# Kernel tuning notes

Measured on AMD Instinct MI355X. Metric: run time of the kernel, lower is better.

Reference implementation:

```python
import jax, jax.numpy as jnp
import numpy as np

D_MODEL = 2048
N_HEADS = 16
HEAD_DIM = D_MODEL // N_HEADS
ROPE_BASE = 10000.0
B, T = 2, 2048


def setup_inputs() -> dict:
    key = jax.random.key(0)
    k1, k2, k3 = jax.random.split(key, 3)
    s_in = 1.0 / np.sqrt(D_MODEL)
    x = jax.random.normal(k1, (B, T, D_MODEL), dtype=jnp.float32)
    Wqkv = jax.random.normal(k2, (3 * D_MODEL, D_MODEL), dtype=jnp.float32) * s_in
    bqkv = jnp.zeros((3 * D_MODEL,), dtype=jnp.float32)
    Wo = jax.random.normal(k3, (D_MODEL, D_MODEL), dtype=jnp.float32) * s_in
    bo = jnp.zeros((D_MODEL,), dtype=jnp.float32)
    return {"x": x, "Wqkv": Wqkv, "bqkv": bqkv, "Wo": Wo, "bo": bo}


def _rotate_half(x):
    # [x1,x2,x3,x4] -> [-x2,x1,-x4,x3] (interleaved pairs)
    x_even = x[..., 0::2]
    x_odd = x[..., 1::2]
    return jnp.stack((-x_odd, x_even), axis=-1).reshape(x.shape)


def _rope_cos_sin(seq_len, dtype):
    half = HEAD_DIM // 2
    inv_freq = 1.0 / (ROPE_BASE ** (jnp.arange(half, dtype=jnp.float32) / half))
    freqs = jnp.arange(seq_len, dtype=jnp.float32)[:, None] * inv_freq[None, :]  # (T, half)
    emb = jnp.repeat(freqs, 2, axis=-1)  # (T, D) interleaved
    cos = jnp.cos(emb).astype(dtype)[None, None]  # (1,1,T,D)
    sin = jnp.sin(emb).astype(dtype)[None, None]
    return cos, sin


def reference(x, Wqkv, bqkv, Wo, bo):
    b, t, c = x.shape
    qkv = jnp.einsum('btc,fc->btf', x, Wqkv) + bqkv  # (B,T,3C)
    q, k, v = jnp.split(qkv, 3, axis=-1)
    def to_heads(z):
        return z.reshape(b, t, N_HEADS, HEAD_DIM).transpose(0, 2, 1, 3)  # (B,H,T,D)
    q, k, v = to_heads(q), to_heads(k), to_heads(v)
    cos, sin = _rope_cos_sin(t, x.dtype)
    q = q * cos + _rotate_half(q) * sin
    k = k * cos + _rotate_half(k) * sin
    scale = 1.0 / jnp.sqrt(jnp.asarray(HEAD_DIM, dtype=x.dtype))
    scores = jnp.einsum('bhqd,bhkd->bhqk', q, k) * scale  # (B,H,T,T)
    causal = jnp.tril(jnp.ones((t, t), dtype=bool))
    scores = jnp.where(causal, scores, jnp.finfo(scores.dtype).min)
    attn = jax.nn.softmax(scores, axis=-1)
    out = jnp.einsum('bhqk,bhkd->bhqd', attn, v)  # (B,H,T,D)
    out = out.transpose(0, 2, 1, 3).reshape(b, t, c)
    return jnp.einsum('btc,oc->bto', out, Wo) + bo
```

## Files before the change

kernel.cpp:

```cpp
#include <hip/hip_runtime.h>

using f16 = _Float16;
typedef _Float16 h8 __attribute__((ext_vector_type(8)));
typedef _Float16 h4 __attribute__((ext_vector_type(4)));
typedef float f4 __attribute__((ext_vector_type(4)));
typedef unsigned int u32;
typedef unsigned long long u64;

#define DEVI static __device__ __forceinline__

DEVI f4 mfma16(h8 a, h8 b, f4 c) {
  return __builtin_amdgcn_mfma_f32_16x16x32_f16(a, b, c, 0, 0, 0);
}

DEVI void gl_lds16(const f16* g, f16* l) {
  __builtin_amdgcn_global_load_lds(
      (const __attribute__((address_space(1))) u32*)g,
      (__attribute__((address_space(3))) u32*)l, 16, 0, 0);
}

DEVI u32 pkh2(float a, float b) {
  union { f16 h[2]; u32 u; } x;
  x.h[0] = (f16)a; x.h[1] = (f16)b;
  return x.u;
}

typedef float fv4 __attribute__((ext_vector_type(4)));

__global__ __launch_bounds__(256) void k_cvt(const float* __restrict__ in,
                                             f16* __restrict__ out, int n4) {
  int i = blockIdx.x * 256 + threadIdx.x;
  if (i >= n4) return;
  fv4 v = ((const fv4*)in)[i];
  h4 o;
  o[0] = (f16)v[0]; o[1] = (f16)v[1]; o[2] = (f16)v[2]; o[3] = (f16)v[3];
  ((h4*)out)[i] = o;
}

__global__ __launch_bounds__(256) void k_rope_tbl(float* __restrict__ tbl) {
  int i = blockIdx.x * 256 + threadIdx.x;
  int t = i >> 6, d = i & 63;
  float invf = exp2f(-(float)d * (13.287712379549449f / 64.f));
  float a = (float)t * invf;
  tbl[2 * i]     = cosf(a);
  tbl[2 * i + 1] = sinf(a);
}

__global__ __launch_bounds__(256) void k_gemm_qkv(const f16* __restrict__ A,
                                                  const f16* __restrict__ Bt,
                                                  const float* __restrict__ bias,
                                                  const float* __restrict__ tbl,
                                                  f16* __restrict__ Qb,
                                                  f16* __restrict__ Kb,
                                                  f16* __restrict__ qkvb,
                                                  int K) {
  __shared__ f16 sA[128 * 64];
  __shared__ f16 sB[128 * 64];
  const int tid = threadIdx.x;
  const int w = tid >> 6, lane = tid & 63;
  const int g = lane >> 4, colq = lane & 15;
  const int wr = w >> 1, wc = w & 1;

  const int nwg = gridDim.x;
  const int q8 = nwg >> 3;
  const int swz = (blockIdx.x & 7) * q8 + (blockIdx.x >> 3);
  const int bm = swz & 31, bn = swz >> 5;

  const f16* Ab = A + (size_t)bm * 128 * K;
  const f16* Bb = Bt + (size_t)bn * 128 * K;
  const int nt = K >> 6;

  const int srow = lane >> 3;
  const int schunk = (lane & 7) ^ srow;
  const int cq7 = colq & 7;

  f4 acc[4][4] = {};
  const int rowA0 = wr * 64 + colq;
  const int rowB0 = wc * 64 + colq;

  for (int t = 0; t < nt; ++t) {
    const int k0 = t << 6;
#pragma unroll
    for (int j = 0; j < 4; ++j) {
      const int r = (w * 4 + j) * 8;
      gl_lds16(Ab + (size_t)(r + srow) * K + k0 + schunk * 8, sA + r * 64);
      gl_lds16(Bb + (size_t)(r + srow) * K + k0 + schunk * 8, sB + r * 64);
    }
    __syncthreads();
    h8 af[2][4], bf[2][4];
#pragma unroll
    for (int kki = 0; kki < 2; ++kki) {
#pragma unroll
      for (int m = 0; m < 4; ++m)
        af[kki][m] = *(const h8*)(sA + (rowA0 + m * 16) * 64 + (((kki * 4 + g) ^ cq7) * 8));
#pragma unroll
      for (int n = 0; n < 4; ++n)
        bf[kki][n] = *(const h8*)(sB + (rowB0 + n * 16) * 64 + (((kki * 4 + g) ^ cq7) * 8));
    }
#pragma unroll
    for (int m = 0; m < 4; ++m)
#pragma unroll
      for (int n = 0; n < 4; ++n)
#pragma unroll
        for (int kki = 0; kki < 2; ++kki)
          acc[m][n] = mfma16(af[kki][m], bf[kki][n], acc[m][n]);
    __syncthreads();
  }

  const int sect = bn >> 4;
  const int h = bn & 15;
  if (sect == 2) {
#pragma unroll
    for (int n = 0; n < 4; ++n) {
      const int col = bn * 128 + wc * 64 + n * 16 + colq;
      const float bv = bias[col];
#pragma unroll
      for (int m = 0; m < 4; ++m) {
        const int row0 = bm * 128 + wr * 64 + m * 16 + 4 * g;
#pragma unroll
        for (int r = 0; r < 4; ++r)
          qkvb[(size_t)(row0 + r) * 6144 + col] = (f16)(acc[m][n][r] + bv);
      }
    }
  } else {
    f16* Out = sect ? Kb : Qb;
    const float SQ = 0.088388347648318447f * 1.4426950408889634f;
    const float scale = sect ? 1.0f : SQ;
    const float2* tbl2 = (const float2*)tbl;
#pragma unroll
    for (int n = 0; n < 4; ++n) {
      const int col = bn * 128 + wc * 64 + n * 16 + colq;
      const int d = col & 127;
      const int dd = d >> 1;
      const bool odd = (d & 1) != 0;
      const float bv = bias[col];
#pragma unroll
      for (int m = 0; m < 4; ++m) {
        const int row0 = bm * 128 + wr * 64 + m * 16 + 4 * g;
#pragma unroll
        for (int r = 0; r < 4; ++r) {
          const int row = row0 + r;
          const int t = row & 2047;
          const int b = row >> 11;
          float v = acc[m][n][r] + bv;
          float p = __shfl_xor(v, 1);
          float2 cs = tbl2[t * 64 + dd];
          float o = odd ? (v * cs.x + p * cs.y) : (v * cs.x - p * cs.y);
          Out[((size_t)(b * 16 + h) * 2048 + t) * 128 + d] = (f16)(o * scale);
        }
      }
    }
  }
}

template <int F32OUT>
__global__ __launch_bounds__(512, 2) void k_gemm128(const f16* __restrict__ A,
                                                    const f16* __restrict__ Bt,
                                                    const float* __restrict__ bias,
                                                    void* __restrict__ Cp,
                                                    int M, int N, int K, int gy) {
  __shared__ f16 lds[2][24576];
  const int tid = threadIdx.x;
  const int w = tid >> 6, lane = tid & 63;
  const int g = lane >> 4, colq = lane & 15;
  const int wr = w >> 2, wc = w & 3;

  const int nwg = gridDim.x;
  const int q8 = nwg >> 3;
  const int swz = (blockIdx.x & 7) * q8 + (blockIdx.x >> 3);
  const int bm = swz % gy, bn = swz / gy;

  const f16* Ab = A + (size_t)bm * 128 * K;
  const f16* Bb = Bt + (size_t)bn * 256 * K;

  const int srow = lane >> 3;
  const int schunk = (lane & 7) ^ srow;
  const int nt = K >> 6;

  auto STAGE = [&](int kt, f16* buf) {
    const int k0 = kt << 6;
    f16* bA = buf;
    f16* bB = buf + 128 * 64;
#pragma unroll
    for (int j = 0; j < 2; ++j) {
      const int r = w * 16 + j * 8;
      gl_lds16(Ab + (size_t)(r + srow) * K + k0 + schunk * 8, bA + r * 64);
    }
#pragma unroll
    for (int j = 0; j < 4; ++j) {
      const int r = w * 32 + j * 8;
      gl_lds16(Bb + (size_t)(r + srow) * K + k0 + schunk * 8, bB + r * 64);
    }
  };

  STAGE(0, lds[0]);
  STAGE(1, lds[1]);
  asm volatile("s_waitcnt vmcnt(6)" ::: "memory");
  __builtin_amdgcn_s_barrier();

  f4 acc[4][4] = {};
  const int rowA0 = wr * 64 + colq;
  const int rowB0 = wc * 64 + colq;
  const int cq7 = colq & 7;

  for (int t = 0; t < nt; ++t) {
    f16* cur = lds[t & 1];
    h8 af[2][4], bf[2][4];
#pragma unroll
    for (int kki = 0; kki < 2; ++kki) {
#pragma unroll
      for (int m = 0; m < 4; ++m)
        af[kki][m] = *(const h8*)(cur + (rowA0 + m * 16) * 64 + (((kki * 4 + g) ^ cq7) * 8));
#pragma unroll
      for (int n = 0; n < 4; ++n)
        bf[kki][n] = *(const h8*)(cur + 8192 + (rowB0 + n * 16) * 64 + (((kki * 4 + g) ^ cq7) * 8));
    }
    asm volatile("s_waitcnt lgkmcnt(0)" ::: "memory");
    __builtin_amdgcn_s_barrier();
    const bool more = (t + 2 < nt);
    if (more) STAGE(t + 2, cur);
    __builtin_amdgcn_s_setprio(1);
#pragma unroll
    for (int m = 0; m < 4; ++m)
#pragma unroll
      for (int n = 0; n < 4; ++n)
#pragma unroll
        for (int kki = 0; kki < 2; ++kki)
          acc[m][n] = mfma16(af[kki][m], bf[kki][n], acc[m][n]);
    __builtin_amdgcn_s_setprio(0);
    if (more) {
      asm volatile("s_waitcnt vmcnt(6)" ::: "memory");
    } else {
      asm volatile("s_waitcnt vmcnt(0)" ::: "memory");
    }
    __builtin_amdgcn_s_barrier();
  }

#pragma unroll
  for (int n = 0; n < 4; ++n) {
    const int col = bn * 256 + wc * 64 + n * 16 + colq;
    const float bv = bias[col];
#pragma unroll
    for (int m = 0; m < 4; ++m) {
      const int row0 = bm * 128 + wr * 64 + m * 16 + 4 * g;
#pragma unroll
      for (int r = 0; r < 4; ++r) {
        float v = acc[m][n][r] + bv;
        if constexpr (F32OUT) {
          ((float*)Cp)[(size_t)(row0 + r) * N + col] = v;
        } else {
          ((f16*)Cp)[(size_t)(row0 + r) * N + col] = (f16)v;
        }
      }
    }
  }
}

__global__ __launch_bounds__(256) void k_vtrans(const f16* __restrict__ qkv,
                                                f16* __restrict__ Vt) {
  __shared__ f16 ldsT[128 * 40];
  const int bh = blockIdx.y, t0 = blockIdx.x * 32;
  const int b = bh >> 4, h = bh & 15;
  const int tid = threadIdx.x;
#pragma unroll
  for (int cc = 0; cc < 2; ++cc) {
    int task = tid + cc * 256;
    int row = task >> 4;
    int ch = task & 15;
    h8 v = *(const h8*)(qkv + (size_t)(b * 2048 + t0 + row) * 6144 + 4096 + h * 128 + ch * 8);
#pragma unroll
    for (int j = 0; j < 8; ++j) ldsT[(ch * 8 + j) * 40 + row] = v[j];
  }
  __syncthreads();
  int d = tid >> 1, seg = tid & 1;
  h8 v0 = *(const h8*)(ldsT + d * 40 + seg * 16);
  h8 v1 = *(const h8*)(ldsT + d * 40 + seg * 16 + 8);
  f16* dst = Vt + ((size_t)bh * 128 + d) * 2048 + t0 + seg * 16;
  *(h8*)dst = v0;
  *(h8*)(dst + 8) = v1;
}

DEVI void stage_tiles(const f16* __restrict__ Kg, const f16* __restrict__ Vtg,
                      f16* bufK, f16* bufV, int kv, int w, int lane) {
#pragma unroll
  for (int jj = 0; jj < 4; ++jj) {
    const int j = w * 4 + jj;
    const int rK = j * 4 + (lane >> 4);
    const int cK = (lane & 15) ^ ((rK & 7) << 1);
    gl_lds16(Kg + (size_t)(kv + rK) * 128 + cK * 8, bufK + j * 512);
    const int rV = j * 8 + (lane >> 3);
    const int cV = (lane & 7) ^ (rV & 7);
    gl_lds16(Vtg + (size_t)rV * 2048 + kv + cV * 8, bufV + j * 512);
  }
}

__global__ __launch_bounds__(256) void k_attn(const f16* __restrict__ Q,
                                              const f16* __restrict__ K,
                                              const f16* __restrict__ Vt,
                                              f16* __restrict__ O) {
  __shared__ f16 lds[2][16384];
  const int tid = threadIdx.x;
  const int w = tid >> 6, lane = tid & 63;
  const int g = lane >> 4, q = lane & 15;
  const int bid = blockIdx.x;
  const int bh = bid & 31;
  const int p = (bid < 256) ? (bid >> 5) : (15 - ((bid - 256) >> 5));

  const f16* Kg = K + (size_t)bh * 2048 * 128;
  const f16* Vtg = Vt + (size_t)bh * 128 * 2048;
  const int qx2 = (q & 7) << 1;
  const int qx = q & 7;

  const int q0w = p * 128 + w * 32;
  const int nit = 2 * (p + 1);

  h8 qf[2][4];
#pragma unroll
  for (int set = 0; set < 2; ++set)
#pragma unroll
    for (int d4 = 0; d4 < 4; ++d4)
      qf[set][d4] = *(const h8*)(Q + ((size_t)bh * 2048 + q0w + 16 * set + q) * 128 + d4 * 32 + g * 8);

  stage_tiles(Kg, Vtg, lds[0], lds[0] + 8192, 0, w, lane);
  asm volatile("s_waitcnt vmcnt(0)" ::: "memory");
  __builtin_amdgcn_s_barrier();

  f4 ot[2][8] = {};
  float mrun[2] = {-3.0e38f, -3.0e38f};
  float lrun[2] = {0.f, 0.f};

  for (int it = 0; it < nit; ++it) {
    const int kv0 = it * 64;
    f16* bufK = lds[it & 1];
    f16* bufV = bufK + 8192;
    if (it + 1 < nit) {
      f16* nb = lds[(it + 1) & 1];
      stage_tiles(Kg, Vtg, nb, nb + 8192, kv0 + 64, w, lane);
    }
    if (kv0 < q0w + 32) {
      f4 st[2][4] = {{{0.f,0.f,0.f,0.f},{0.f,0.f,0.f,0.f},{0.f,0.f,0.f,0.f},{0.f,0.f,0.f,0.f}},
                     {{0.f,0.f,0.f,0.f},{0.f,0.f,0.f,0.f},{0.f,0.f,0.f,0.f},{0.f,0.f,0.f,0.f}}};
#pragma unroll
      for (int d4 = 0; d4 < 4; ++d4) {
        h8 kf[4];
#pragma unroll
        for (int s = 0; s < 4; ++s)
          kf[s] = *(const h8*)(bufK + ((16 * s + q) * 16 + ((4 * d4 + g) ^ qx2)) * 8);
#pragma unroll
        for (int set = 0; set < 2; ++set)
#pragma unroll
          for (int s = 0; s < 4; ++s)
            st[set][s] = mfma16(kf[s], qf[set][d4], st[set][s]);
      }
      if (kv0 + 63 > q0w) {
#pragma unroll
        for (int set = 0; set < 2; ++set) {
          const int qcol = q0w + 16 * set + q;
#pragma unroll
          for (int s = 0; s < 4; ++s)
#pragma unroll
            for (int r = 0; r < 4; ++r)
              if (kv0 + s * 16 + 4 * g + r > qcol) st[set][s][r] = -3.0e38f;
        }
      }
      float pm[2];
#pragma unroll
      for (int set = 0; set < 2; ++set) {
        float m0 = st[set][0][0];
#pragma unroll
        for (int s = 0; s < 4; ++s)
#pragma unroll
          for (int r = 0; r < 4; ++r) m0 = fmaxf(m0, st[set][s][r]);
        m0 = fmaxf(m0, __shfl_xor(m0, 16));
        m0 = fmaxf(m0, __shfl_xor(m0, 32));
        pm[set] = m0;
      }
      const bool ok = (pm[0] <= mrun[0] + 8.0f) && (pm[1] <= mrun[1] + 8.0f);
      if (!__all(ok)) {
#pragma unroll
        for (int set = 0; set < 2; ++set) {
          float mnew = fmaxf(mrun[set], pm[set]);
          float corr = exp2f(mrun[set] - mnew);
          lrun[set] *= corr;
#pragma unroll
          for (int dt = 0; dt < 8; ++dt) ot[set][dt] *= corr;
          mrun[set] = mnew;
        }
      }
#pragma unroll
      for (int set = 0; set < 2; ++set) {
        float ps = 0.f;
#pragma unroll
        for (int s = 0; s < 4; ++s)
#pragma unroll
          for (int r = 0; r < 4; ++r) {
            st[set][s][r] = exp2f(st[set][s][r] - mrun[set]);
            ps += st[set][s][r];
          }
        ps += __shfl_xor(ps, 16);
        ps += __shfl_xor(ps, 32);
        lrun[set] += ps;
      }
      union { u32 u[4]; h8 h; } pb[2][2];
      const int s0l = ((g & 1) << 5) | q;
      const bool hi = g >= 2;
#pragma unroll
      for (int set = 0; set < 2; ++set)
#pragma unroll
        for (int hh = 0; hh < 2; ++hh) {
          u32 wA0 = pkh2(st[set][2 * hh][0], st[set][2 * hh][1]);
          u32 wB0 = pkh2(st[set][2 * hh][2], st[set][2 * hh][3]);
          u32 wA1 = pkh2(st[set][2 * hh + 1][0], st[set][2 * hh + 1][1]);
          u32 wB1 = pkh2(st[set][2 * hh + 1][2], st[set][2 * hh + 1][3]);
          u32 a0 = (u32)__shfl((int)wA0, s0l),      a1 = (u32)__shfl((int)wA1, s0l);
          u32 b0 = (u32)__shfl((int)wB0, s0l),      b1 = (u32)__shfl((int)wB1, s0l);
          u32 c0 = (u32)__shfl((int)wA0, s0l + 16), c1 = (u32)__shfl((int)wA1, s0l + 16);
          u32 d0 = (u32)__shfl((int)wB0, s0l + 16), d1 = (u32)__shfl((int)wB1, s0l + 16);
          pb[set][hh].u[0] = hi ? a1 : a0;
          pb[set][hh].u[1] = hi ? b1 : b0;
          pb[set][hh].u[2] = hi ? c1 : c0;
          pb[set][hh].u[3] = hi ? d1 : d0;
        }
#pragma unroll
      for (int hh = 0; hh < 2; ++hh)
#pragma unroll
        for (int dt = 0; dt < 8; ++dt) {
          h8 vf = *(const h8*)(bufV + ((dt * 16 + q) * 8 + ((4 * hh + g) ^ qx)) * 8);
#pragma unroll
          for (int set = 0; set < 2; ++set)
            ot[set][dt] = mfma16(vf, pb[set][hh].h, ot[set][dt]);
        }
    }
    asm volatile("s_waitcnt vmcnt(0)" ::: "memory");
    __builtin_amdgcn_s_barrier();
  }

#pragma unroll
  for (int set = 0; set < 2; ++set) {
    float linv = 1.0f / lrun[set];
    f16* Ob = O + ((size_t)(bh >> 4) * 2048 + q0w + 16 * set + q) * 2048 + (bh & 15) * 128 + 4 * g;
#pragma unroll
    for (int dt = 0; dt < 8; ++dt) {
      union { f16 hh4[4]; u64 u; } o;
#pragma unroll
      for (int r = 0; r < 4; ++r) o.hh4[r] = (f16)(ot[set][dt][r] * linv);
      *(u64*)(Ob + dt * 16) = o.u;
    }
  }
}

extern "C" void kernel_launch(void* const* d_in, const int* in_sizes, int n_in,
                              void* d_out, int out_size, void* d_ws, size_t ws_size,
                              hipStream_t stream) {
  (void)in_sizes; (void)n_in; (void)out_size; (void)ws_size;
  const float* x    = (const float*)d_in[0];
  const float* Wqkv = (const float*)d_in[1];
  const float* bqkv = (const float*)d_in[2];
  const float* Wo   = (const float*)d_in[3];
  const float* bo   = (const float*)d_in[4];

  char* ws = (char*)d_ws;
  f16* xb    = (f16*)ws; ws += (size_t)4096 * 2048 * 2;
  f16* wqkvb = (f16*)ws; ws += (size_t)6144 * 2048 * 2;
  f16* wob   = (f16*)ws; ws += (size_t)2048 * 2048 * 2;
  f16* qkvb  = (f16*)ws; ws += (size_t)4096 * 6144 * 2;
  f16* Qb    = (f16*)ws; ws += (size_t)32 * 2048 * 128 * 2;
  f16* Kb    = (f16*)ws; ws += (size_t)32 * 2048 * 128 * 2;
  f16* Vtb   = (f16*)ws; ws += (size_t)32 * 128 * 2048 * 2;
  f16* attb  = (f16*)ws; ws += (size_t)4096 * 2048 * 2;
  float* tbl = (float*)ws; ws += (size_t)2048 * 64 * 2 * 4;

  k_cvt<<<8192, 256, 0, stream>>>(x, xb, 2097152);
  k_cvt<<<12288, 256, 0, stream>>>(Wqkv, wqkvb, 3145728);
  k_cvt<<<4096, 256, 0, stream>>>(Wo, wob, 1048576);
  k_rope_tbl<<<512, 256, 0, stream>>>(tbl);

  k_gemm_qkv<<<1536, 256, 0, stream>>>(xb, wqkvb, bqkv, tbl, Qb, Kb, qkvb, 2048);

  k_vtrans<<<dim3(64, 32), 256, 0, stream>>>(qkvb, Vtb);

  k_attn<<<512, 256, 0, stream>>>(Qb, Kb, Vtb, attb);

  k_gemm128<1><<<256, 512, 0, stream>>>(attb, wob, bo, d_out, 4096, 2048, 2048, 32);
}
```

Baseline: 313.8 us.

## Fuse V transpose into QKV GEMM epilogue and pack Q/K rope stores

The QKV GEMM epilogue now writes the V section directly in transposed (B,H,D,T) layout, packing four consecutive time steps into one 64-bit store. This removes the intermediate qkv buffer and the separate k_vtrans kernel launch along with its global round trip. The Q/K rope epilogue also has even lanes compute both elements of each pair and write one packed 32-bit store, halving store instructions. The transposed V writes are strided by 2048 elements per lane, which may coalesce less well than the previous row-major writes.

```diff
diff --git a/kernel.cpp b/kernel.cpp
--- a/kernel.cpp
+++ b/kernel.cpp
@@ -52,7 +52,7 @@
                                                   const float* __restrict__ tbl,
                                                   f16* __restrict__ Qb,
                                                   f16* __restrict__ Kb,
-                                                  f16* __restrict__ qkvb,
+                                                  f16* __restrict__ Vtb,
                                                   int K) {
   __shared__ f16 sA[128 * 64];
   __shared__ f16 sB[128 * 64];
@@ -110,16 +110,20 @@
   const int sect = bn >> 4;
   const int h = bn & 15;
   if (sect == 2) {
+    const int bq = bm >> 4;
+    const int tblk = (bm * 128) & 2047;
 #pragma unroll
     for (int n = 0; n < 4; ++n) {
-      const int col = bn * 128 + wc * 64 + n * 16 + colq;
-      const float bv = bias[col];
+      const int d = wc * 64 + n * 16 + colq;
+      const float bv = bias[4096 + h * 128 + d];
+      f16* vbase = Vtb + ((size_t)(bq * 16 + h) * 128 + d) * 2048;
 #pragma unroll
       for (int m = 0; m < 4; ++m) {
-        const int row0 = bm * 128 + wr * 64 + m * 16 + 4 * g;
-#pragma unroll
-        for (int r = 0; r < 4; ++r)
-          qkvb[(size_t)(row0 + r) * 6144 + col] = (f16)(acc[m][n][r] + bv);
+        const int t0m = tblk + wr * 64 + m * 16 + 4 * g;
+        union { f16 x[4]; u64 u; } vv;
+#pragma unroll
+        for (int r = 0; r < 4; ++r) vv.x[r] = (f16)(acc[m][n][r] + bv);
+        *(u64*)(vbase + t0m) = vv.u;
       }
     }
   } else {
@@ -127,12 +131,12 @@
     const float SQ = 0.088388347648318447f * 1.4426950408889634f;
     const float scale = sect ? 1.0f : SQ;
     const float2* tbl2 = (const float2*)tbl;
+    const bool evenl = (colq & 1) == 0;
 #pragma unroll
     for (int n = 0; n < 4; ++n) {
       const int col = bn * 128 + wc * 64 + n * 16 + colq;
       const int d = col & 127;
       const int dd = d >> 1;
-      const bool odd = (d & 1) != 0;
       const float bv = bias[col];
 #pragma unroll
       for (int m = 0; m < 4; ++m) {
@@ -145,8 +149,10 @@
           float v = acc[m][n][r] + bv;
           float p = __shfl_xor(v, 1);
           float2 cs = tbl2[t * 64 + dd];
-          float o = odd ? (v * cs.x + p * cs.y) : (v * cs.x - p * cs.y);
-          Out[((size_t)(b * 16 + h) * 2048 + t) * 128 + d] = (f16)(o * scale);
+          float oe = (v * cs.x - p * cs.y) * scale;
+          float oo = (p * cs.x + v * cs.y) * scale;
+          if (evenl)
+            *(u32*)(Out + ((size_t)(b * 16 + h) * 2048 + t) * 128 + d) = pkh2(oe, oo);
         }
       }
     }
@@ -254,30 +260,6 @@
       }
     }
   }
-}
-
-__global__ __launch_bounds__(256) void k_vtrans(const f16* __restrict__ qkv,
-                                                f16* __restrict__ Vt) {
-  __shared__ f16 ldsT[128 * 40];
-  const int bh = blockIdx.y, t0 = blockIdx.x * 32;
-  const int b = bh >> 4, h = bh & 15;
-  const int tid = threadIdx.x;
-#pragma unroll
-  for (int cc = 0; cc < 2; ++cc) {
-    int task = tid + cc * 256;
-    int row = task >> 4;
-    int ch = task & 15;
-    h8 v = *(const h8*)(qkv + (size_t)(b * 2048 + t0 + row) * 6144 + 4096 + h * 128 + ch * 8);
-#pragma unroll
-    for (int j = 0; j < 8; ++j) ldsT[(ch * 8 + j) * 40 + row] = v[j];
-  }
-  __syncthreads();
-  int d = tid >> 1, seg = tid & 1;
-  h8 v0 = *(const h8*)(ldsT + d * 40 + seg * 16);
-  h8 v1 = *(const h8*)(ldsT + d * 40 + seg * 16 + 8);
-  f16* dst = Vt + ((size_t)bh * 128 + d) * 2048 + t0 + seg * 16;
-  *(h8*)dst = v0;
-  *(h8*)(dst + 8) = v1;
 }
 
 DEVI void stage_tiles(const f16* __restrict__ Kg, const f16* __restrict__ Vtg,
@@ -463,7 +445,6 @@
   f16* xb    = (f16*)ws; ws += (size_t)4096 * 2048 * 2;
   f16* wqkvb = (f16*)ws; ws += (size_t)6144 * 2048 * 2;
   f16* wob   = (f16*)ws; ws += (size_t)2048 * 2048 * 2;
-  f16* qkvb  = (f16*)ws; ws += (size_t)4096 * 6144 * 2;
   f16* Qb    = (f16*)ws; ws += (size_t)32 * 2048 * 128 * 2;
   f16* Kb    = (f16*)ws; ws += (size_t)32 * 2048 * 128 * 2;
   f16* Vtb   = (f16*)ws; ws += (size_t)32 * 128 * 2048 * 2;
@@ -475,9 +456,7 @@
   k_cvt<<<4096, 256, 0, stream>>>(Wo, wob, 1048576);
   k_rope_tbl<<<512, 256, 0, stream>>>(tbl);
 
-  k_gemm_qkv<<<1536, 256, 0, stream>>>(xb, wqkvb, bqkv, tbl, Qb, Kb, qkvb, 2048);
-
-  k_vtrans<<<dim3(64, 32), 256, 0, stream>>>(qkvb, Vtb);
+  k_gemm_qkv<<<1536, 256, 0, stream>>>(xb, wqkvb, bqkv, tbl, Qb, Kb, Vtb, 2048);
 
   k_attn<<<512, 256, 0, stream>>>(Qb, Kb, Vtb, attb);
 
```

New measurement: 325.5 us. 1.04x slower.

## Halve attention query tile, load V directly from global, fuse prep kernels

Applied to the files above, without the earlier changes.

The attention kernel now handles 64 query rows per block (16 per wave) instead of 128, doubling the grid to 1024 blocks. A new causal pairing maps blocks to balanced query tiles. V fragments are read straight from global memory rather than staged in LDS, which halves LDS use but relies on cache hits for V reuse. The three fp32->fp16 conversion launches and the RoPE table launch are merged into one kernel to cut launch overhead. The trade-off is more K reloads per head and uncoalesced, unpipelined global V loads inside the inner loop, in exchange for more parallelism and occupancy.

```diff
diff --git a/kernel.cpp b/kernel.cpp
--- a/kernel.cpp
+++ b/kernel.cpp
@@ -27,23 +27,31 @@
 
 typedef float fv4 __attribute__((ext_vector_type(4)));
 
-__global__ __launch_bounds__(256) void k_cvt(const float* __restrict__ in,
-                                             f16* __restrict__ out, int n4) {
+__global__ __launch_bounds__(256) void k_prep(const float* __restrict__ x,
+                                              const float* __restrict__ wqkv,
+                                              const float* __restrict__ wo,
+                                              f16* __restrict__ xb,
+                                              f16* __restrict__ wqkvb,
+                                              f16* __restrict__ wob,
+                                              float* __restrict__ tbl) {
   int i = blockIdx.x * 256 + threadIdx.x;
-  if (i >= n4) return;
-  fv4 v = ((const fv4*)in)[i];
-  h4 o;
-  o[0] = (f16)v[0]; o[1] = (f16)v[1]; o[2] = (f16)v[2]; o[3] = (f16)v[3];
-  ((h4*)out)[i] = o;
-}
-
-__global__ __launch_bounds__(256) void k_rope_tbl(float* __restrict__ tbl) {
-  int i = blockIdx.x * 256 + threadIdx.x;
-  int t = i >> 6, d = i & 63;
-  float invf = exp2f(-(float)d * (13.287712379549449f / 64.f));
-  float a = (float)t * invf;
-  tbl[2 * i]     = cosf(a);
-  tbl[2 * i + 1] = sinf(a);
+  if (i < 6291456) {
+    const float* src; f16* dst; int off;
+    if (i < 2097152)      { src = x;    dst = xb;    off = i; }
+    else if (i < 5242880) { src = wqkv; dst = wqkvb; off = i - 2097152; }
+    else                  { src = wo;   dst = wob;   off = i - 5242880; }
+    fv4 v = ((const fv4*)src)[off];
+    h4 o;
+    o[0] = (f16)v[0]; o[1] = (f16)v[1]; o[2] = (f16)v[2]; o[3] = (f16)v[3];
+    ((h4*)dst)[off] = o;
+  } else {
+    int i2 = i - 6291456;
+    int t = i2 >> 6, d = i2 & 63;
+    float invf = exp2f(-(float)d * (13.287712379549449f / 64.f));
+    float a = (float)t * invf;
+    tbl[2 * i2]     = cosf(a);
+    tbl[2 * i2 + 1] = sinf(a);
+  }
 }
 
 __global__ __launch_bounds__(256) void k_gemm_qkv(const f16* __restrict__ A,
@@ -280,17 +288,13 @@
   *(h8*)(dst + 8) = v1;
 }
 
-DEVI void stage_tiles(const f16* __restrict__ Kg, const f16* __restrict__ Vtg,
-                      f16* bufK, f16* bufV, int kv, int w, int lane) {
+DEVI void stage_K(const f16* __restrict__ Kg, f16* bufK, int kv, int w, int lane) {
 #pragma unroll
   for (int jj = 0; jj < 4; ++jj) {
     const int j = w * 4 + jj;
     const int rK = j * 4 + (lane >> 4);
     const int cK = (lane & 15) ^ ((rK & 7) << 1);
     gl_lds16(Kg + (size_t)(kv + rK) * 128 + cK * 8, bufK + j * 512);
-    const int rV = j * 8 + (lane >> 3);
-    const int cV = (lane & 7) ^ (rV & 7);
-    gl_lds16(Vtg + (size_t)rV * 2048 + kv + cV * 8, bufV + j * 512);
   }
 }
 
@@ -298,48 +302,42 @@
                                               const f16* __restrict__ K,
                                               const f16* __restrict__ Vt,
                                               f16* __restrict__ O) {
-  __shared__ f16 lds[2][16384];
+  __shared__ f16 lds[2][8192];
   const int tid = threadIdx.x;
   const int w = tid >> 6, lane = tid & 63;
   const int g = lane >> 4, q = lane & 15;
   const int bid = blockIdx.x;
   const int bh = bid & 31;
-  const int p = (bid < 256) ? (bid >> 5) : (15 - ((bid - 256) >> 5));
+  const int k4 = bid >> 8;
+  const int r = (bid >> 5) & 7;
+  const int p = (k4 == 0) ? (2 * r) : (k4 == 1) ? (2 * r + 1)
+              : (k4 == 2) ? (31 - 2 * r) : (30 - 2 * r);
 
   const f16* Kg = K + (size_t)bh * 2048 * 128;
-  const f16* Vtg = Vt + (size_t)bh * 128 * 2048;
+  const f16* Vb = Vt + ((size_t)bh * 128 + q) * 2048 + g * 8;
   const int qx2 = (q & 7) << 1;
-  const int qx = q & 7;
-
-  const int q0w = p * 128 + w * 32;
-  const int nit = 2 * (p + 1);
-
-  h8 qf[2][4];
-#pragma unroll
-  for (int set = 0; set < 2; ++set)
-#pragma unroll
-    for (int d4 = 0; d4 < 4; ++d4)
-      qf[set][d4] = *(const h8*)(Q + ((size_t)bh * 2048 + q0w + 16 * set + q) * 128 + d4 * 32 + g * 8);
-
-  stage_tiles(Kg, Vtg, lds[0], lds[0] + 8192, 0, w, lane);
+
+  const int q0w = p * 64 + w * 16;
+  const int nit = p + 1;
+
+  h8 qf[4];
+#pragma unroll
+  for (int d4 = 0; d4 < 4; ++d4)
+    qf[d4] = *(const h8*)(Q + ((size_t)bh * 2048 + q0w + q) * 128 + d4 * 32 + g * 8);
+
+  stage_K(Kg, lds[0], 0, w, lane);
   asm volatile("s_waitcnt vmcnt(0)" ::: "memory");
   __builtin_amdgcn_s_barrier();
 
-  f4 ot[2][8] = {};
-  float mrun[2] = {-3.0e38f, -3.0e38f};
-  float lrun[2] = {0.f, 0.f};
+  f4 ot[8] = {};
+  float mrun = -3.0e38f, lrun = 0.f;
 
   for (int it = 0; it < nit; ++it) {
     const int kv0 = it * 64;
     f16* bufK = lds[it & 1];
-    f16* bufV = bufK + 8192;
-    if (it + 1 < nit) {
-      f16* nb = lds[(it + 1) & 1];
-      stage_tiles(Kg, Vtg, nb, nb + 8192, kv0 + 64, w, lane);
-    }
-    if (kv0 < q0w + 32) {
-      f4 st[2][4] = {{{0.f,0.f,0.f,0.f},{0.f,0.f,0.f,0.f},{0.f,0.f,0.f,0.f},{0.f,0.f,0.f,0.f}},
-                     {{0.f,0.f,0.f,0.f},{0.f,0.f,0.f,0.f},{0.f,0.f,0.f,0.f},{0.f,0.f,0.f,0.f}}};
+    if (it + 1 < nit) stage_K(Kg, lds[(it + 1) & 1], kv0 + 64, w, lane);
+    if (kv0 < q0w + 16) {
+      f4 st[4] = {{0.f,0.f,0.f,0.f},{0.f,0.f,0.f,0.f},{0.f,0.f,0.f,0.f},{0.f,0.f,0.f,0.f}};
 #pragma unroll
       for (int d4 = 0; d4 < 4; ++d4) {
         h8 kf[4];
@@ -347,105 +345,82 @@
         for (int s = 0; s < 4; ++s)
           kf[s] = *(const h8*)(bufK + ((16 * s + q) * 16 + ((4 * d4 + g) ^ qx2)) * 8);
 #pragma unroll
-        for (int set = 0; set < 2; ++set)
-#pragma unroll
-          for (int s = 0; s < 4; ++s)
-            st[set][s] = mfma16(kf[s], qf[set][d4], st[set][s]);
+        for (int s = 0; s < 4; ++s)
+          st[s] = mfma16(kf[s], qf[d4], st[s]);
       }
       if (kv0 + 63 > q0w) {
-#pragma unroll
-        for (int set = 0; set < 2; ++set) {
-          const int qcol = q0w + 16 * set + q;
-#pragma unroll
-          for (int s = 0; s < 4; ++s)
-#pragma unroll
-            for (int r = 0; r < 4; ++r)
-              if (kv0 + s * 16 + 4 * g + r > qcol) st[set][s][r] = -3.0e38f;
+        const int qcol = q0w + q;
+#pragma unroll
+        for (int s = 0; s < 4; ++s)
+#pragma unroll
+          for (int rr = 0; rr < 4; ++rr)
+            if (kv0 + s * 16 + 4 * g + rr > qcol) st[s][rr] = -3.0e38f;
+      }
+      float pm = st[0][0];
+#pragma unroll
+      for (int s = 0; s < 4; ++s)
+#pragma unroll
+        for (int rr = 0; rr < 4; ++rr) pm = fmaxf(pm, st[s][rr]);
+      pm = fmaxf(pm, __shfl_xor(pm, 16));
+      pm = fmaxf(pm, __shfl_xor(pm, 32));
+      if (!__all(pm <= mrun + 8.0f)) {
+        float mnew = fmaxf(mrun, pm);
+        float corr = exp2f(mrun - mnew);
+        lrun *= corr;
+#pragma unroll
+        for (int dt = 0; dt < 8; ++dt) ot[dt] *= corr;
+        mrun = mnew;
+      }
+      float ps = 0.f;
+#pragma unroll
+      for (int s = 0; s < 4; ++s)
+#pragma unroll
+        for (int rr = 0; rr < 4; ++rr) {
+          st[s][rr] = exp2f(st[s][rr] - mrun);
+          ps += st[s][rr];
         }
-      }
-      float pm[2];
-#pragma unroll
-      for (int set = 0; set < 2; ++set) {
-        float m0 = st[set][0][0];
-#pragma unroll
-        for (int s = 0; s < 4; ++s)
-#pragma unroll
-          for (int r = 0; r < 4; ++r) m0 = fmaxf(m0, st[set][s][r]);
-        m0 = fmaxf(m0, __shfl_xor(m0, 16));
-        m0 = fmaxf(m0, __shfl_xor(m0, 32));
-        pm[set] = m0;
-      }
-      const bool ok = (pm[0] <= mrun[0] + 8.0f) && (pm[1] <= mrun[1] + 8.0f);
-      if (!__all(ok)) {
-#pragma unroll
-        for (int set = 0; set < 2; ++set) {
-          float mnew = fmaxf(mrun[set], pm[set]);
-          float corr = exp2f(mrun[set] - mnew);
-          lrun[set] *= corr;
-#pragma unroll
-          for (int dt = 0; dt < 8; ++dt) ot[set][dt] *= corr;
-          mrun[set] = mnew;
-        }
-      }
-#pragma unroll
-      for (int set = 0; set < 2; ++set) {
-        float ps = 0.f;
-#pragma unroll
-        for (int s = 0; s < 4; ++s)
-#pragma unroll
-          for (int r = 0; r < 4; ++r) {
-            st[set][s][r] = exp2f(st[set][s][r] - mrun[set]);
-            ps += st[set][s][r];
-          }
-        ps += __shfl_xor(ps, 16);
-        ps += __shfl_xor(ps, 32);
-        lrun[set] += ps;
-      }
-      union { u32 u[4]; h8 h; } pb[2][2];
+      ps += __shfl_xor(ps, 16);
+      ps += __shfl_xor(ps, 32);
+      lrun += ps;
+
+      union { u32 u[4]; h8 h; } pb[2];
       const int s0l = ((g & 1) << 5) | q;
       const bool hi = g >= 2;
 #pragma unroll
-      for (int set = 0; set < 2; ++set)
-#pragma unroll
-        for (int hh = 0; hh < 2; ++hh) {
-          u32 wA0 = pkh2(st[set][2 * hh][0], st[set][2 * hh][1]);
-          u32 wB0 = pkh2(st[set][2 * hh][2], st[set][2 * hh][3]);
-          u32 wA1 = pkh2(st[set][2 * hh + 1][0], st[set][2 * hh + 1][1]);
-          u32 wB1 = pkh2(st[set][2 * hh + 1][2], st[set][2 * hh + 1][3]);
-          u32 a0 = (u32)__shfl((int)wA0, s0l),      a1 = (u32)__shfl((int)wA1, s0l);
-          u32 b0 = (u32)__shfl((int)wB0, s0l),      b1 = (u32)__shfl((int)wB1, s0l);
-          u32 c0 = (u32)__shfl((int)wA0, s0l + 16), c1 = (u32)__shfl((int)wA1, s0l + 16);
-          u32 d0 = (u32)__shfl((int)wB0, s0l + 16), d1 = (u32)__shfl((int)wB1, s0l + 16);
-          pb[set][hh].u[0] = hi ? a1 : a0;
-          pb[set][hh].u[1] = hi ? b1 : b0;
-          pb[set][hh].u[2] = hi ? c1 : c0;
-          pb[set][hh].u[3] = hi ? d1 : d0;
-        }
+      for (int hh = 0; hh < 2; ++hh) {
+        u32 wA0 = pkh2(st[2 * hh][0], st[2 * hh][1]);
+        u32 wB0 = pkh2(st[2 * hh][2], st[2 * hh][3]);
+        u32 wA1 = pkh2(st[2 * hh + 1][0], st[2 * hh + 1][1]);
+        u32 wB1 = pkh2(st[2 * hh + 1][2], st[2 * hh + 1][3]);
+        u32 a0 = (u32)__shfl((int)wA0, s0l),      a1 = (u32)__shfl((int)wA1, s0l);
+        u32 b0 = (u32)__shfl((int)wB0, s0l),      b1 = (u32)__shfl((int)wB1, s0l);
+        u32 c0 = (u32)__shfl((int)wA0, s0l + 16), c1 = (u32)__shfl((int)wA1, s0l + 16);
+        u32 d0 = (u32)__shfl((int)wB0, s0l + 16), d1 = (u32)__shfl((int)wB1, s0l + 16);
+        pb[hh].u[0] = hi ? a1 : a0;
+        pb[hh].u[1] = hi ? b1 : b0;
+        pb[hh].u[2] = hi ? c1 : c0;
+        pb[hh].u[3] = hi ? d1 : d0;
+      }
 #pragma unroll
       for (int hh = 0; hh < 2; ++hh)
 #pragma unroll
         for (int dt = 0; dt < 8; ++dt) {
-          h8 vf = *(const h8*)(bufV + ((dt * 16 + q) * 8 + ((4 * hh + g) ^ qx)) * 8);
-#pragma unroll
-          for (int set = 0; set < 2; ++set)
-            ot[set][dt] = mfma16(vf, pb[set][hh].h, ot[set][dt]);
+          h8 vf = *(const h8*)(Vb + (size_t)dt * 16 * 2048 + kv0 + hh * 32);
+          ot[dt] = mfma16(vf, pb[hh].h, ot[dt]);
         }
     }
     asm volatile("s_waitcnt vmcnt(0)" ::: "memory");
     __builtin_amdgcn_s_barrier();
   }
 
-#pragma unroll
-  for (int set = 0; set < 2; ++set) {
-    float linv = 1.0f / lrun[set];
-    f16* Ob = O + ((size_t)(bh >> 4) * 2048 + q0w + 16 * set + q) * 2048 + (bh & 15) * 128 + 4 * g;
-#pragma unroll
-    for (int dt = 0; dt < 8; ++dt) {
-      union { f16 hh4[4]; u64 u; } o;
-#pragma unroll
-      for (int r = 0; r < 4; ++r) o.hh4[r] = (f16)(ot[set][dt][r] * linv);
-      *(u64*)(Ob + dt * 16) = o.u;
-    }
+  float linv = 1.0f / lrun;
+  f16* Ob = O + ((size_t)(bh >> 4) * 2048 + q0w + q) * 2048 + (bh & 15) * 128 + 4 * g;
+#pragma unroll
+  for (int dt = 0; dt < 8; ++dt) {
+    union { f16 hh4[4]; u64 u; } o;
+#pragma unroll
+    for (int rr = 0; rr < 4; ++rr) o.hh4[rr] = (f16)(ot[dt][rr] * linv);
+    *(u64*)(Ob + dt * 16) = o.u;
   }
 }
 
@@ -470,16 +445,13 @@
   f16* attb  = (f16*)ws; ws += (size_t)4096 * 2048 * 2;
   float* tbl = (float*)ws; ws += (size_t)2048 * 64 * 2 * 4;
 
-  k_cvt<<<8192, 256, 0, stream>>>(x, xb, 2097152);
-  k_cvt<<<12288, 256, 0, stream>>>(Wqkv, wqkvb, 3145728);
-  k_cvt<<<4096, 256, 0, stream>>>(Wo, wob, 1048576);
-  k_rope_tbl<<<512, 256, 0, stream>>>(tbl);
+  k_prep<<<25088, 256, 0, stream>>>(x, Wqkv, Wo, xb, wqkvb, wob, tbl);
 
   k_gemm_qkv<<<1536, 256, 0, stream>>>(xb, wqkvb, bqkv, tbl, Qb, Kb, qkvb, 2048);
 
   k_vtrans<<<dim3(64, 32), 256, 0, stream>>>(qkvb, Vtb);
 
-  k_attn<<<512, 256, 0, stream>>>(Qb, Kb, Vtb, attb);
+  k_attn<<<1024, 256, 0, stream>>>(Qb, Kb, Vtb, attb);
 
   k_gemm128<1><<<256, 512, 0, stream>>>(attb, wob, bo, d_out, 4096, 2048, 2048, 32);
 }
```

Measured after the change: 404.9 us. +29.1%, slower.
